# Kernel optimization log

Hardware: AMD Instinct MI355X
Metric: run time of the kernel (lower is better)

## Reference

```python
import jax, jax.numpy as jnp
import numpy as np

B, TWO_N, D, DK = 256, 4096, 3, 64


def setup_inputs() -> dict:
    key = jax.random.key(0)
    ks = jax.random.split(key, 7)
    inp = jax.random.normal(ks[0], (B, TWO_N, D), dtype=jnp.float32)
    # nn.Linear params, stored as [in, out] so y = x @ W + b
    Wq = jax.random.normal(ks[1], (D, DK), dtype=jnp.float32) / np.sqrt(D)
    bq = jax.random.normal(ks[2], (DK,), dtype=jnp.float32) * 0.01
    Wk = jax.random.normal(ks[3], (D, DK), dtype=jnp.float32) / np.sqrt(D)
    bk = jax.random.normal(ks[4], (DK,), dtype=jnp.float32) * 0.01
    Wv = jax.random.normal(ks[5], (D, D), dtype=jnp.float32) / np.sqrt(D)
    bv = jax.random.normal(ks[6], (D,), dtype=jnp.float32) * 0.01
    return {"input": inp, "Wq": Wq, "bq": bq, "Wk": Wk, "bk": bk, "Wv": Wv, "bv": bv}


def _efficient_attention(x, Wq, bq, Wk, bk, Wv, bv):
    # x: [B, N, D]
    q = jax.nn.softmax(x @ Wq + bq, axis=2)   # softmax over d_k
    k = jax.nn.softmax(x @ Wk + bk, axis=1)   # softmax over sequence N
    v = x @ Wv + bv                            # [B, N, D]
    context = jnp.einsum('bnk,bnv->bkv', k, v)  # [B, DK, D]
    out = jnp.einsum('bnk,bkv->bnv', q, context)  # [B, N, D]
    return jnp.mean(out, axis=1, keepdims=True)   # [B, 1, D]


def reference(input, Wq, bq, Wk, bk, Wv, bv):
    # detach=True in original: stop gradient through the input
    inp = jax.lax.stop_gradient(input)
    x, y = jnp.split(inp, 2, axis=1)
    ax = _efficient_attention(x, Wq, bq, Wk, bk, Wv, bv)
    ay = _efficient_attention(y, Wq, bq, Wk, bk, Wv, bv)
    a = (ax + ay) * 0.5
    a = a / jnp.sqrt(jnp.sum(a * a, axis=2, keepdims=True))
    return a
```

## Files before the change

### kernel.cpp

```cpp
#include <hip/hip_runtime.h>
#include <math.h>

#define BATCH 256
#define NHALF 2048
#define DIN 3
#define DK 64
#define SPLIT 4
#define ROWS_PER_BLOCK (NHALF / SPLIT)
#define ROWS_PER_WAVE  (ROWS_PER_BLOCK / 4)

__global__ __launch_bounds__(256) void ea_partial(
    const float* __restrict__ inp,
    const float* __restrict__ Wq, const float* __restrict__ bq,
    const float* __restrict__ Wk, const float* __restrict__ bk,
    const float* __restrict__ Wv, const float* __restrict__ bv,
    float* __restrict__ ws)
{
    const int blk   = blockIdx.x;
    const int b     = blk / (2 * SPLIT);
    const int rem   = blk % (2 * SPLIT);
    const int half  = rem / SPLIT;
    const int slice = rem % SPLIT;

    const int tid  = threadIdx.x;
    const int w    = tid >> 6;
    const int lane = tid & 63;
    const int g    = lane >> 4;
    const int sub  = lane & 15;

    float wq0[4], wq1[4], wq2[4], bqv[4];
    float wk0[4], wk1[4], wk2[4], bkv[4];
#pragma unroll
    for (int j = 0; j < 4; ++j) {
        int k = sub + 16 * j;
        wq0[j] = Wq[0 * DK + k]; wq1[j] = Wq[1 * DK + k]; wq2[j] = Wq[2 * DK + k];
        bqv[j] = bq[k];
        wk0[j] = Wk[0 * DK + k]; wk1[j] = Wk[1 * DK + k]; wk2[j] = Wk[2 * DK + k];
        bkv[j] = bk[k];
    }
    float wv[9], bvv[3];
#pragma unroll
    for (int i = 0; i < 9; ++i) wv[i] = Wv[i];
#pragma unroll
    for (int i = 0; i < 3; ++i) bvv[i] = bv[i];

    float accq[4] = {0.f, 0.f, 0.f, 0.f};
    float ek[4]   = {0.f, 0.f, 0.f, 0.f};
    float ekv[4][3] = {{0.f,0.f,0.f},{0.f,0.f,0.f},{0.f,0.f,0.f},{0.f,0.f,0.f}};

    const float* xbase = inp + ((size_t)b * (2 * NHALF) + (size_t)half * NHALF) * DIN;
    const int row0 = slice * ROWS_PER_BLOCK + w * ROWS_PER_WAVE;

    for (int i = 0; i < ROWS_PER_WAVE; i += 4) {
        const int row = row0 + i + g;
        const float* xp = xbase + (size_t)row * DIN;
        const float x0 = xp[0], x1 = xp[1], x2 = xp[2];

        const float v0 = fmaf(x0, wv[0], fmaf(x1, wv[3], fmaf(x2, wv[6], bvv[0])));
        const float v1 = fmaf(x0, wv[1], fmaf(x1, wv[4], fmaf(x2, wv[7], bvv[1])));
        const float v2 = fmaf(x0, wv[2], fmaf(x1, wv[5], fmaf(x2, wv[8], bvv[2])));

        float eq[4];
        float rowsum = 0.f;
#pragma unroll
        for (int j = 0; j < 4; ++j) {
            float sq = fmaf(x0, wq0[j], fmaf(x1, wq1[j], fmaf(x2, wq2[j], bqv[j])));
            eq[j] = __expf(sq);
            rowsum += eq[j];
        }
        rowsum += __shfl_xor(rowsum, 1);
        rowsum += __shfl_xor(rowsum, 2);
        rowsum += __shfl_xor(rowsum, 4);
        rowsum += __shfl_xor(rowsum, 8);
        const float inv = __builtin_amdgcn_rcpf(rowsum);

#pragma unroll
        for (int j = 0; j < 4; ++j) {
            accq[j] = fmaf(eq[j], inv, accq[j]);
            float sk = fmaf(x0, wk0[j], fmaf(x1, wk1[j], fmaf(x2, wk2[j], bkv[j])));
            float e = __expf(sk);
            ek[j] += e;
            ekv[j][0] = fmaf(e, v0, ekv[j][0]);
            ekv[j][1] = fmaf(e, v1, ekv[j][1]);
            ekv[j][2] = fmaf(e, v2, ekv[j][2]);
        }
    }

    __shared__ float lds[16][321];
    const int slot = w * 4 + g;
#pragma unroll
    for (int j = 0; j < 4; ++j) {
        int k = sub + 16 * j;
        lds[slot][k]        = accq[j];
        lds[slot][64 + k]   = ek[j];
        lds[slot][128 + k]  = ekv[j][0];
        lds[slot][192 + k]  = ekv[j][1];
        lds[slot][256 + k]  = ekv[j][2];
    }
    __syncthreads();

    float* outp = ws + (size_t)blk * 320;
    for (int idx = tid; idx < 320; idx += 256) {
        float s = 0.f;
#pragma unroll
        for (int p = 0; p < 16; ++p) s += lds[p][idx];
        outp[idx] = s;
    }
}

__global__ __launch_bounds__(64) void ea_final(
    const float* __restrict__ ws, float* __restrict__ out)
{
    const int b = blockIdx.x;
    const int lane = threadIdx.x;

    float res[2][3];
#pragma unroll
    for (int h = 0; h < 2; ++h) {
        float accq = 0.f, ek = 0.f, e0 = 0.f, e1 = 0.f, e2 = 0.f;
#pragma unroll
        for (int s = 0; s < SPLIT; ++s) {
            const float* p = ws + (size_t)((b * 2 + h) * SPLIT + s) * 320;
            accq += p[lane];
            ek   += p[64 + lane];
            e0   += p[128 + lane];
            e1   += p[192 + lane];
            e2   += p[256 + lane];
        }
        const float mq = accq * (1.0f / (float)NHALF);
        const float r  = mq / ek;
        float p0 = r * e0, p1 = r * e1, p2 = r * e2;
        for (int m = 1; m < 64; m <<= 1) {
            p0 += __shfl_xor(p0, m);
            p1 += __shfl_xor(p1, m);
            p2 += __shfl_xor(p2, m);
        }
        res[h][0] = p0; res[h][1] = p1; res[h][2] = p2;
    }

    const float a0 = 0.5f * (res[0][0] + res[1][0]);
    const float a1 = 0.5f * (res[0][1] + res[1][1]);
    const float a2 = 0.5f * (res[0][2] + res[1][2]);
    const float nrm = rsqrtf(a0 * a0 + a1 * a1 + a2 * a2);
    if (lane == 0) {
        out[(size_t)b * 3 + 0] = a0 * nrm;
        out[(size_t)b * 3 + 1] = a1 * nrm;
        out[(size_t)b * 3 + 2] = a2 * nrm;
    }
}

extern "C" void kernel_launch(void* const* d_in, const int* in_sizes, int n_in,
                              void* d_out, int out_size, void* d_ws, size_t ws_size,
                              hipStream_t stream) {
    const float* inp = (const float*)d_in[0];
    const float* Wq  = (const float*)d_in[1];
    const float* bq  = (const float*)d_in[2];
    const float* Wk  = (const float*)d_in[3];
    const float* bk  = (const float*)d_in[4];
    const float* Wv  = (const float*)d_in[5];
    const float* bv  = (const float*)d_in[6];
    float* ws  = (float*)d_ws;
    float* out = (float*)d_out;

    hipLaunchKernelGGL(ea_partial, dim3(BATCH * 2 * SPLIT), dim3(256), 0, stream,
                       inp, Wq, bq, Wk, bk, Wv, bv, ws);
    hipLaunchKernelGGL(ea_final, dim3(BATCH), dim3(64), 0, stream, ws, out);
}
```

Baseline: 113.8 us.

## Fuse partial and final kernels via atomic last-block reduction, defer V projection

Merges the two kernels into one: each block writes its partial sums, bumps a per-batch atomic counter, and the last block for that batch does the final reduction and normalisation. The value projection moves out of the inner loop by accumulating exp(k)·x and applying Wv/bv once at the end. Other changes: pre-scaling weights by log2(e) so exp2 can be used, processing two rows per iteration, and cross-group shuffle reduction instead of a 16-slot LDS reduction. This adds a memset launch and threadfence/atomic synchronisation.

```diff
diff --git a/kernel.cpp b/kernel.cpp
--- a/kernel.cpp
+++ b/kernel.cpp
@@ -3,24 +3,30 @@
 
 #define BATCH 256
 #define NHALF 2048
-#define DIN 3
 #define DK 64
 #define SPLIT 4
+#define NBLK (BATCH * 2 * SPLIT)
 #define ROWS_PER_BLOCK (NHALF / SPLIT)
 #define ROWS_PER_WAVE  (ROWS_PER_BLOCK / 4)
+#define PART_STRIDE 320
+#define CNT_OFF_BYTES ((size_t)NBLK * PART_STRIDE * 4)
 
-__global__ __launch_bounds__(256) void ea_partial(
+__device__ __forceinline__ float rcp_fast(float x)  { return __builtin_amdgcn_rcpf(x); }
+__device__ __forceinline__ float exp2_fast(float x) { return __builtin_amdgcn_exp2f(x); }
+
+__global__ __launch_bounds__(256) void ea_fused(
     const float* __restrict__ inp,
     const float* __restrict__ Wq, const float* __restrict__ bq,
     const float* __restrict__ Wk, const float* __restrict__ bk,
     const float* __restrict__ Wv, const float* __restrict__ bv,
-    float* __restrict__ ws)
+    float* __restrict__ ws, unsigned* __restrict__ cnt,
+    float* __restrict__ out)
 {
     const int blk   = blockIdx.x;
-    const int b     = blk / (2 * SPLIT);
-    const int rem   = blk % (2 * SPLIT);
-    const int half  = rem / SPLIT;
-    const int slice = rem % SPLIT;
+    const int b     = blk >> 3;
+    const int rem   = blk & 7;
+    const int half  = rem >> 2;
+    const int slice = rem & 3;
 
     const int tid  = threadIdx.x;
     const int w    = tid >> 6;
@@ -28,124 +34,138 @@
     const int g    = lane >> 4;
     const int sub  = lane & 15;
 
+    const float LOG2E = 1.4426950408889634f;
     float wq0[4], wq1[4], wq2[4], bqv[4];
     float wk0[4], wk1[4], wk2[4], bkv[4];
 #pragma unroll
     for (int j = 0; j < 4; ++j) {
         int k = sub + 16 * j;
-        wq0[j] = Wq[0 * DK + k]; wq1[j] = Wq[1 * DK + k]; wq2[j] = Wq[2 * DK + k];
-        bqv[j] = bq[k];
-        wk0[j] = Wk[0 * DK + k]; wk1[j] = Wk[1 * DK + k]; wk2[j] = Wk[2 * DK + k];
-        bkv[j] = bk[k];
+        wq0[j] = Wq[k] * LOG2E; wq1[j] = Wq[64 + k] * LOG2E; wq2[j] = Wq[128 + k] * LOG2E;
+        bqv[j] = bq[k] * LOG2E;
+        wk0[j] = Wk[k] * LOG2E; wk1[j] = Wk[64 + k] * LOG2E; wk2[j] = Wk[128 + k] * LOG2E;
+        bkv[j] = bk[k] * LOG2E;
     }
-    float wv[9], bvv[3];
-#pragma unroll
-    for (int i = 0; i < 9; ++i) wv[i] = Wv[i];
-#pragma unroll
-    for (int i = 0; i < 3; ++i) bvv[i] = bv[i];
 
-    float accq[4] = {0.f, 0.f, 0.f, 0.f};
-    float ek[4]   = {0.f, 0.f, 0.f, 0.f};
-    float ekv[4][3] = {{0.f,0.f,0.f},{0.f,0.f,0.f},{0.f,0.f,0.f},{0.f,0.f,0.f}};
+    float accq[4] = {0,0,0,0}, ek[4] = {0,0,0,0};
+    float ex0[4] = {0,0,0,0}, ex1[4] = {0,0,0,0}, ex2[4] = {0,0,0,0};
 
-    const float* xbase = inp + ((size_t)b * (2 * NHALF) + (size_t)half * NHALF) * DIN;
-    const int row0 = slice * ROWS_PER_BLOCK + w * ROWS_PER_WAVE;
+    const float* xp = inp
+        + ((size_t)b * (2 * NHALF) + (size_t)half * NHALF
+           + (size_t)slice * ROWS_PER_BLOCK + (size_t)w * ROWS_PER_WAVE + g) * 3;
 
-    for (int i = 0; i < ROWS_PER_WAVE; i += 4) {
-        const int row = row0 + i + g;
-        const float* xp = xbase + (size_t)row * DIN;
-        const float x0 = xp[0], x1 = xp[1], x2 = xp[2];
+    for (int i = 0; i < ROWS_PER_WAVE; i += 8) {
+        const float a0 = xp[0],  a1 = xp[1],  a2 = xp[2];
+        const float c0 = xp[12], c1 = xp[13], c2 = xp[14];
+        xp += 24;
 
-        const float v0 = fmaf(x0, wv[0], fmaf(x1, wv[3], fmaf(x2, wv[6], bvv[0])));
-        const float v1 = fmaf(x0, wv[1], fmaf(x1, wv[4], fmaf(x2, wv[7], bvv[1])));
-        const float v2 = fmaf(x0, wv[2], fmaf(x1, wv[5], fmaf(x2, wv[8], bvv[2])));
-
-        float eq[4];
-        float rowsum = 0.f;
+        float eqA[4], eqB[4];
+        float rsA = 0.f, rsB = 0.f;
 #pragma unroll
         for (int j = 0; j < 4; ++j) {
-            float sq = fmaf(x0, wq0[j], fmaf(x1, wq1[j], fmaf(x2, wq2[j], bqv[j])));
-            eq[j] = __expf(sq);
-            rowsum += eq[j];
+            eqA[j] = exp2_fast(fmaf(a0, wq0[j], fmaf(a1, wq1[j], fmaf(a2, wq2[j], bqv[j]))));
+            rsA += eqA[j];
+            eqB[j] = exp2_fast(fmaf(c0, wq0[j], fmaf(c1, wq1[j], fmaf(c2, wq2[j], bqv[j]))));
+            rsB += eqB[j];
         }
-        rowsum += __shfl_xor(rowsum, 1);
-        rowsum += __shfl_xor(rowsum, 2);
-        rowsum += __shfl_xor(rowsum, 4);
-        rowsum += __shfl_xor(rowsum, 8);
-        const float inv = __builtin_amdgcn_rcpf(rowsum);
+        rsA += __shfl_xor(rsA, 1);  rsB += __shfl_xor(rsB, 1);
+        rsA += __shfl_xor(rsA, 2);  rsB += __shfl_xor(rsB, 2);
+        rsA += __shfl_xor(rsA, 4);  rsB += __shfl_xor(rsB, 4);
+        rsA += __shfl_xor(rsA, 8);  rsB += __shfl_xor(rsB, 8);
+        const float invA = rcp_fast(rsA);
+        const float invB = rcp_fast(rsB);
 
 #pragma unroll
         for (int j = 0; j < 4; ++j) {
-            accq[j] = fmaf(eq[j], inv, accq[j]);
-            float sk = fmaf(x0, wk0[j], fmaf(x1, wk1[j], fmaf(x2, wk2[j], bkv[j])));
-            float e = __expf(sk);
-            ek[j] += e;
-            ekv[j][0] = fmaf(e, v0, ekv[j][0]);
-            ekv[j][1] = fmaf(e, v1, ekv[j][1]);
-            ekv[j][2] = fmaf(e, v2, ekv[j][2]);
+            accq[j] = fmaf(eqA[j], invA, fmaf(eqB[j], invB, accq[j]));
+            float eA = exp2_fast(fmaf(a0, wk0[j], fmaf(a1, wk1[j], fmaf(a2, wk2[j], bkv[j]))));
+            float eB = exp2_fast(fmaf(c0, wk0[j], fmaf(c1, wk1[j], fmaf(c2, wk2[j], bkv[j]))));
+            ek[j]  += eA + eB;
+            ex0[j] = fmaf(eA, a0, fmaf(eB, c0, ex0[j]));
+            ex1[j] = fmaf(eA, a1, fmaf(eB, c1, ex1[j]));
+            ex2[j] = fmaf(eA, a2, fmaf(eB, c2, ex2[j]));
         }
     }
 
-    __shared__ float lds[16][321];
-    const int slot = w * 4 + g;
 #pragma unroll
     for (int j = 0; j < 4; ++j) {
-        int k = sub + 16 * j;
-        lds[slot][k]        = accq[j];
-        lds[slot][64 + k]   = ek[j];
-        lds[slot][128 + k]  = ekv[j][0];
-        lds[slot][192 + k]  = ekv[j][1];
-        lds[slot][256 + k]  = ekv[j][2];
+        accq[j] += __shfl_xor(accq[j], 16); accq[j] += __shfl_xor(accq[j], 32);
+        ek[j]   += __shfl_xor(ek[j], 16);   ek[j]   += __shfl_xor(ek[j], 32);
+        ex0[j]  += __shfl_xor(ex0[j], 16);  ex0[j]  += __shfl_xor(ex0[j], 32);
+        ex1[j]  += __shfl_xor(ex1[j], 16);  ex1[j]  += __shfl_xor(ex1[j], 32);
+        ex2[j]  += __shfl_xor(ex2[j], 16);  ex2[j]  += __shfl_xor(ex2[j], 32);
+    }
+
+    __shared__ float lds[4][PART_STRIDE];
+    __shared__ int isLast;
+    if (g == 0) {
+#pragma unroll
+        for (int j = 0; j < 4; ++j) {
+            int k = sub + 16 * j;
+            lds[w][k]       = accq[j];
+            lds[w][64 + k]  = ek[j];
+            lds[w][128 + k] = ex0[j];
+            lds[w][192 + k] = ex1[j];
+            lds[w][256 + k] = ex2[j];
+        }
     }
     __syncthreads();
 
-    float* outp = ws + (size_t)blk * 320;
-    for (int idx = tid; idx < 320; idx += 256) {
-        float s = 0.f;
+    float* op = ws + (size_t)blk * PART_STRIDE;
+    for (int idx = tid; idx < PART_STRIDE; idx += 256)
+        op[idx] = lds[0][idx] + lds[1][idx] + lds[2][idx] + lds[3][idx];
+
+    __threadfence();
+    __syncthreads();
+    if (tid == 0) {
+        unsigned old = __hip_atomic_fetch_add(&cnt[b], 1u, __ATOMIC_ACQ_REL,
+                                              __HIP_MEMORY_SCOPE_AGENT);
+        isLast = (old == 2 * SPLIT - 1) ? 1 : 0;
+    }
+    __syncthreads();
+
+    if (isLast && tid < 64) {
+        __threadfence();
+        float wv[9], bvv[3];
 #pragma unroll
-        for (int p = 0; p < 16; ++p) s += lds[p][idx];
-        outp[idx] = s;
-    }
-}
+        for (int i = 0; i < 9; ++i) wv[i] = Wv[i];
+#pragma unroll
+        for (int i = 0; i < 3; ++i) bvv[i] = bv[i];
 
-__global__ __launch_bounds__(64) void ea_final(
-    const float* __restrict__ ws, float* __restrict__ out)
-{
-    const int b = blockIdx.x;
-    const int lane = threadIdx.x;
-
-    float res[2][3];
+        const float* basep = ws + (size_t)b * (2 * SPLIT) * PART_STRIDE;
+        float res[2][3];
 #pragma unroll
-    for (int h = 0; h < 2; ++h) {
-        float accq = 0.f, ek = 0.f, e0 = 0.f, e1 = 0.f, e2 = 0.f;
+        for (int h = 0; h < 2; ++h) {
+            float aq = 0.f, ekk = 0.f, e0 = 0.f, e1 = 0.f, e2 = 0.f;
 #pragma unroll
-        for (int s = 0; s < SPLIT; ++s) {
-            const float* p = ws + (size_t)((b * 2 + h) * SPLIT + s) * 320;
-            accq += p[lane];
-            ek   += p[64 + lane];
-            e0   += p[128 + lane];
-            e1   += p[192 + lane];
-            e2   += p[256 + lane];
+            for (int s = 0; s < SPLIT; ++s) {
+                const float* p = basep + (size_t)(h * SPLIT + s) * PART_STRIDE;
+                aq  += p[tid];
+                ekk += p[64 + tid];
+                e0  += p[128 + tid];
+                e1  += p[192 + tid];
+                e2  += p[256 + tid];
+            }
+            const float r = aq / ((float)NHALF * ekk);
+            float c0 = fmaf(e0, wv[0], fmaf(e1, wv[3], fmaf(e2, wv[6], bvv[0] * ekk)));
+            float c1 = fmaf(e0, wv[1], fmaf(e1, wv[4], fmaf(e2, wv[7], bvv[1] * ekk)));
+            float c2 = fmaf(e0, wv[2], fmaf(e1, wv[5], fmaf(e2, wv[8], bvv[2] * ekk)));
+            float p0 = r * c0, p1 = r * c1, p2 = r * c2;
+            for (int m = 1; m < 64; m <<= 1) {
+                p0 += __shfl_xor(p0, m);
+                p1 += __shfl_xor(p1, m);
+                p2 += __shfl_xor(p2, m);
+            }
+            res[h][0] = p0; res[h][1] = p1; res[h][2] = p2;
         }
-        const float mq = accq * (1.0f / (float)NHALF);
-        const float r  = mq / ek;
-        float p0 = r * e0, p1 = r * e1, p2 = r * e2;
-        for (int m = 1; m < 64; m <<= 1) {
-            p0 += __shfl_xor(p0, m);
-            p1 += __shfl_xor(p1, m);
-            p2 += __shfl_xor(p2, m);
+        const float a0 = 0.5f * (res[0][0] + res[1][0]);
+        const float a1 = 0.5f * (res[0][1] + res[1][1]);
+        const float a2 = 0.5f * (res[0][2] + res[1][2]);
+        const float nrm = rsqrtf(fmaf(a0, a0, fmaf(a1, a1, a2 * a2)));
+        if (tid == 0) {
+            out[(size_t)b * 3 + 0] = a0 * nrm;
+            out[(size_t)b * 3 + 1] = a1 * nrm;
+            out[(size_t)b * 3 + 2] = a2 * nrm;
         }
-        res[h][0] = p0; res[h][1] = p1; res[h][2] = p2;
-    }
-
-    const float a0 = 0.5f * (res[0][0] + res[1][0]);
-    const float a1 = 0.5f * (res[0][1] + res[1][1]);
-    const float a2 = 0.5f * (res[0][2] + res[1][2]);
-    const float nrm = rsqrtf(a0 * a0 + a1 * a1 + a2 * a2);
-    if (lane == 0) {
-        out[(size_t)b * 3 + 0] = a0 * nrm;
-        out[(size_t)b * 3 + 1] = a1 * nrm;
-        out[(size_t)b * 3 + 2] = a2 * nrm;
     }
 }
 
@@ -159,10 +179,11 @@
     const float* bk  = (const float*)d_in[4];
     const float* Wv  = (const float*)d_in[5];
     const float* bv  = (const float*)d_in[6];
-    float* ws  = (float*)d_ws;
-    float* out = (float*)d_out;
+    float*    ws  = (float*)d_ws;
+    unsigned* cnt = (unsigned*)((char*)d_ws + CNT_OFF_BYTES);
+    float*    out = (float*)d_out;
 
-    hipLaunchKernelGGL(ea_partial, dim3(BATCH * 2 * SPLIT), dim3(256), 0, stream,
-                       inp, Wq, bq, Wk, bk, Wv, bv, ws);
-    hipLaunchKernelGGL(ea_final, dim3(BATCH), dim3(64), 0, stream, ws, out);
+    hipMemsetAsync(cnt, 0, BATCH * sizeof(unsigned), stream);
+    hipLaunchKernelGGL(ea_fused, dim3(NBLK), dim3(256), 0, stream,
+                       inp, Wq, bq, Wk, bk, Wv, bv, ws, cnt, out);
 }
```

New measurement: 308.6 us. +171.2%, slower.
